# Kernel optimization log

Measured on AMD Instinct MI355X. Metric: run time of the kernel, lower is better.

Reference implementation:

```python
import jax, jax.numpy as jnp
import numpy as np

N_NODES = 10000
N_EDGES = 160000
B = 128
HEADS = 4
DIMS = [36, 128, 256, 512]
NEG_SLOPE = 0.2  # PyG GATConv default


def setup_inputs() -> dict:
    key = jax.random.key(0)
    ks = jax.random.split(key, 32)
    inp = {}
    inp["x"] = jax.random.normal(ks[0], (N_NODES, DIMS[0]), jnp.float32)
    inp["edge_index"] = jax.random.randint(ks[1], (2, N_EDGES), 0, N_NODES)
    inp["batch"] = jnp.sort(jax.random.randint(ks[2], (N_NODES,), 0, B))
    ki = 3
    for i in range(3):
        din, dout = DIMS[i], DIMS[i + 1]
        C = dout // HEADS
        inp[f"gcn_w{i}"] = jax.random.normal(ks[ki], (din, dout), jnp.float32) * (din ** -0.5); ki += 1
        inp[f"gcn_b{i}"] = jnp.zeros((dout,), jnp.float32)
        inp[f"gat_w{i}"] = jax.random.normal(ks[ki], (dout, dout), jnp.float32) * (dout ** -0.5); ki += 1
        inp[f"gat_as{i}"] = jax.random.normal(ks[ki], (HEADS, C), jnp.float32) * 0.1; ki += 1
        inp[f"gat_ad{i}"] = jax.random.normal(ks[ki], (HEADS, C), jnp.float32) * 0.1; ki += 1
        inp[f"gat_b{i}"] = jnp.zeros((dout,), jnp.float32)
    D = DIMS[-1]
    inp["ap_w1"] = jax.random.normal(ks[ki], (D, D // 2), jnp.float32) * (D ** -0.5); ki += 1
    inp["ap_b1"] = jnp.zeros((D // 2,), jnp.float32)
    inp["ap_w2"] = jax.random.normal(ks[ki], (D // 2, 1), jnp.float32) * ((D // 2) ** -0.5); ki += 1
    inp["ap_b2"] = jnp.zeros((1,), jnp.float32)
    return inp


def _gcn(x, w, b, src, dst, n):
    # PyG GCNConv: add self-loops, symmetric deg^-1/2 normalization, bias after agg
    h = x @ w  # [N, dout]
    deg = jax.ops.segment_sum(jnp.ones_like(dst, dtype=h.dtype), dst, n) + 1.0  # incl. self-loop
    dinv = deg ** -0.5
    norm = dinv[src] * dinv[dst]  # [E]
    agg = jax.ops.segment_sum(h[src] * norm[:, None], dst, n)
    agg = agg + h * (dinv * dinv)[:, None]  # self-loop messages
    return agg + b


def _gat(x, w, a_s, a_d, b, src, dst, n):
    # PyG GATConv: self-loops, leaky-relu logits, segment softmax over dst, concat heads
    C = w.shape[1] // HEADS
    h = (x @ w).reshape(n, HEADS, C)
    alpha_src = (h * a_s).sum(-1)  # [N, H]
    alpha_dst = (h * a_d).sum(-1)  # [N, H]
    loop = jnp.arange(n)
    s = jnp.concatenate([src, loop])
    d = jnp.concatenate([dst, loop])
    e = jax.nn.leaky_relu(alpha_src[s] + alpha_dst[d], NEG_SLOPE)  # [E+N, H]
    m = jax.ops.segment_max(e, d, n)
    ex = jnp.exp(e - m[d])
    den = jax.ops.segment_sum(ex, d, n)
    alpha = ex / den[d]  # [E+N, H]
    out = jax.ops.segment_sum(h[s] * alpha[:, :, None], d, n)  # [N, H, C]
    return out.reshape(n, HEADS * C) + b


def _forward(x, edge_index, batch, params, ap_w1, ap_b1, ap_w2, ap_b2):
    src, dst = edge_index[0], edge_index[1]
    n = x.shape[0]
    x_in = x
    n_layers = len(params)
    for i, (gw, gb, aw, a_s, a_d, ab) in enumerate(params):
        h = jax.nn.relu(_gcn(x, gw, gb, src, dst, n))  # dropout is identity in eval
        x = h + _gat(h, aw, a_s, a_d, ab, src, dst, n)
        if i < n_layers - 1:
            if x.shape[-1] == x_in.shape[-1]:
                x = x + x_in
            x_in = x
    # attention pooling (global softmax then per-graph masked renorm)
    a = jnp.tanh(x @ ap_w1 + ap_b1) @ ap_w2 + ap_b2  # [N, 1]
    a = jax.nn.softmax(a, axis=0)
    mask = jax.nn.one_hot(batch, B, dtype=x.dtype)  # [N, B]
    aw_ = a * mask
    aw_ = aw_ / (aw_.sum(0, keepdims=True) + 1e-8)
    graph_emb = aw_.T @ x  # [B, D]
    cnt = jax.ops.segment_sum(jnp.ones((n,), x.dtype), batch, B)
    ssum = jax.ops.segment_sum(x, batch, B)
    mean = ssum / jnp.maximum(cnt, 1.0)[:, None]
    smax = jax.ops.segment_max(x, batch, B)
    return jnp.concatenate([graph_emb, mean, smax, ssum], axis=1)  # [B, 4*D]


def reference(x, edge_index, batch,
              gcn_w0, gcn_b0, gat_w0, gat_as0, gat_ad0, gat_b0,
              gcn_w1, gcn_b1, gat_w1, gat_as1, gat_ad1, gat_b1,
              gcn_w2, gcn_b2, gat_w2, gat_as2, gat_ad2, gat_b2,
              ap_w1, ap_b1, ap_w2, ap_b2):
    params = [
        (gcn_w0, gcn_b0, gat_w0, gat_as0, gat_ad0, gat_b0),
        (gcn_w1, gcn_b1, gat_w1, gat_as1, gat_ad1, gat_b1),
        (gcn_w2, gcn_b2, gat_w2, gat_as2, gat_ad2, gat_b2),
    ]
    return _forward(x, edge_index, batch, params, ap_w1, ap_b1, ap_w2, ap_b2)
```

## Files before the change

### kernel.cpp

```cpp
#include <hip/hip_runtime.h>
#include <math.h>

#define NN 10000
#define NE 160000
#define NB 128
#define NH 4
#define DOUT 512
#define NEG 0.2f
#define CNT_BLKS ((NE + 255) / 256)

typedef __attribute__((ext_vector_type(8))) short short8;
typedef __attribute__((ext_vector_type(4))) float f32x4;
typedef __attribute__((ext_vector_type(4))) unsigned short us4;

__device__ __forceinline__ float leakyf(float v){ return v > 0.f ? v : NEG*v; }
__device__ __forceinline__ void fma4(float4& a, const float4 v, float w){
  a.x += v.x*w; a.y += v.y*w; a.z += v.z*w; a.w += v.w*w;
}
__device__ __forceinline__ void mul4(float4& a, float s){
  a.x *= s; a.y *= s; a.z *= s; a.w *= s;
}
__device__ __forceinline__ unsigned short f2bf(float f){
  unsigned int u = __float_as_uint(f);
  u += 0x7FFFu + ((u >> 16) & 1u);
  return (unsigned short)(u >> 16);
}
__device__ __forceinline__ float bf2f(unsigned short h){
  return __uint_as_float(((unsigned int)h) << 16);
}
__device__ __forceinline__ void split2(float v, unsigned short& h, unsigned short& l){
  h = f2bf(v);
  l = f2bf(v - bf2f(h));
}
__device__ __forceinline__ void store_hl(unsigned short* H, unsigned short* L,
                                         size_t base, float4 v){
  us4 h, l; unsigned short hh, ll;
  split2(v.x, hh, ll); h[0]=hh; l[0]=ll;
  split2(v.y, hh, ll); h[1]=hh; l[1]=ll;
  split2(v.z, hh, ll); h[2]=hh; l[2]=ll;
  split2(v.w, hh, ll); h[3]=hh; l[3]=ll;
  *(us4*)&H[base] = h;
  *(us4*)&L[base] = l;
}
__device__ __forceinline__ float4 load_hl(const unsigned short* __restrict__ H,
                                          const unsigned short* __restrict__ L, size_t base){
  us4 h = *(const us4*)&H[base];
  us4 l = *(const us4*)&L[base];
  return make_float4(bf2f(h[0])+bf2f(l[0]), bf2f(h[1])+bf2f(l[1]),
                     bf2f(h[2])+bf2f(l[2]), bf2f(h[3])+bf2f(l[3]));
}
__device__ __forceinline__ void gl_lds16(const unsigned short* g, unsigned short* l){
  __builtin_amdgcn_global_load_lds(
      (const __attribute__((address_space(1))) unsigned int*)g,
      (__attribute__((address_space(3))) unsigned int*)l, 16, 0, 0);
}

struct AllConv {
  const float* src[7];
  unsigned short* dh[7];
  unsigned short* dl[7];
  int K[7], Mm[7], Kp[7], tot[7];
};

__global__ void k_count_conv(const int* __restrict__ dst, int* __restrict__ cnt,
                             AllConv a, int convTot){
  int bid = blockIdx.x;
  if (bid < CNT_BLKS){
    int e = bid*256 + threadIdx.x;
    if (e < NE) atomicAdd(&cnt[dst[e]], 1);
  } else {
    int idx = (bid - CNT_BLKS)*256 + threadIdx.x;
    if (idx >= convTot) return;
    int j = 0;
    while (idx >= a.tot[j]){ idx -= a.tot[j]; j++; }
    int Kp = a.Kp[j], K = a.K[j], M = a.Mm[j];
    int kk = idx % Kp, m = idx / Kp;
    float v = (kk < K) ? a.src[j][(size_t)kk*M + m] : 0.f;
    unsigned short h, l; split2(v, h, l);
    a.dh[j][idx] = h; a.dl[j][idx] = l;
  }
}

__global__ __launch_bounds__(1024) void k_scan_all(
    const int* __restrict__ cnt, const int* __restrict__ batch,
    int* __restrict__ rowptr, float* __restrict__ dinv,
    int* __restrict__ cursor, float* __restrict__ apre,
    int* __restrict__ starts){
  __shared__ int sh[NN];
  __shared__ int pref[1024];
  int t = threadIdx.x;
  for (int i = t; i < NN; i += 1024) sh[i] = cnt[i];
  if (t <= NB){
    int lo = 0, hi = NN;
    while (lo < hi){ int mid = (lo + hi) >> 1; if (batch[mid] < t) lo = mid + 1; else hi = mid; }
    starts[t] = lo;
  }
  __syncthreads();
  int base = t*10;
  int csum = 0;
#pragma unroll
  for (int k = 0; k < 10; k++){ int i = base + k; if (i < NN) csum += sh[i]; }
  pref[t] = csum; __syncthreads();
  for (int o = 1; o < 1024; o <<= 1){
    int v = (t >= o) ? pref[t - o] : 0;
    __syncthreads();
    pref[t] += v;
    __syncthreads();
  }
  int run = pref[t] - csum;
#pragma unroll
  for (int k = 0; k < 10; k++){
    int i = base + k;
    if (i < NN){
      int c = sh[i];
      rowptr[i] = run;
      run += c;
      dinv[i] = rsqrtf((float)c + 1.f);
      cursor[i] = 0;
      apre[i] = 0.f;
    }
  }
  if (t == 1023) rowptr[NN] = pref[1023];
}

__global__ void k_fill(const int* __restrict__ src, const int* __restrict__ dst,
                       const int* __restrict__ rowptr, int* __restrict__ cursor,
                       int* __restrict__ colidx){
  int e = blockIdx.x*blockDim.x + threadIdx.x;
  if (e >= NE) return;
  int d = dst[e];
  int pos = atomicAdd(&cursor[d], 1);
  colidx[rowptr[d] + pos] = src[e];
}

#define GBM 64
#define GBN 128
#define GBK 64
__global__ __launch_bounds__(256) void k_gemm_bf3(
    const unsigned short* __restrict__ Ah, const unsigned short* __restrict__ Al,
    const unsigned short* __restrict__ Bh, const unsigned short* __restrict__ Bl,
    float* __restrict__ C, int N, int Kp, int M, int mode,
    const float* __restrict__ bias, unsigned short* __restrict__ outH,
    unsigned short* __restrict__ outL,
    const float* __restrict__ a_s, const float* __restrict__ a_d,
    float* __restrict__ as_o, float* __restrict__ ad_o, int Cdim){
  __shared__ unsigned short AsH[2*GBM*32], AsL[2*GBM*32];
  __shared__ unsigned short BsH[2*GBN*32], BsL[2*GBN*32];
  __shared__ float sred[2][GBM][4];
  int gx = M / GBN;
  int gy = (N + GBM - 1) / GBM;
  const int G = 8;
  int bid = blockIdx.x;
  int full = gy / G;
  int bid_full = full * G * gx;
  int by, bx;
  if (bid < bid_full){
    int g = bid / (G*gx); int rem = bid % (G*gx);
    by = g*G + rem % G; bx = rem / G;
  } else {
    int rem = bid - bid_full; int rows = gy - full*G;
    by = full*G + rem % rows; bx = rem / rows;
  }
  int row0 = by * GBM, col0 = bx * GBN;
  int t = threadIdx.x;
  int w = t >> 6, L = t & 63;
  int lm = L & 15, lq = L >> 4;
  int wc = w * 32;

  int sr = L >> 2, sc = L & 3;
  int art = w*16 + sr;
  int ga  = (sc - ((art >> 1) & 3)) & 3;
  int agrow = min(row0 + art, N-1);
  int brt0 = w*16 + sr;
  int brt1 = (w+4)*16 + sr;
  int gb0 = (sc - ((brt0 >> 1) & 3)) & 3;
  int gb1 = (sc - ((brt1 >> 1) & 3)) & 3;
  int bgrow0 = col0 + brt0, bgrow1 = col0 + brt1;

  int rc = (lq + (lm >> 1)) & 3;
  int aoff[4], boff[2];
#pragma unroll
  for (int mi = 0; mi < 4; mi++) aoff[mi] = (mi*16 + lm)*32 + rc*8;
#pragma unroll
  for (int ni = 0; ni < 2; ni++) boff[ni] = (wc + ni*16 + lm)*32 + rc*8;

  f32x4 acc[4][2];
#pragma unroll
  for (int i = 0; i < 4; i++)
#pragma unroll
    for (int j = 0; j < 2; j++) acc[i][j] = (f32x4){0.f,0.f,0.f,0.f};

  int nk = Kp / GBK;
  for (int kt = 0; kt < nk; kt++){
    int k0 = kt * GBK;
    if (kt) __syncthreads();
#pragma unroll
    for (int h = 0; h < 2; h++){
      int kh = k0 + h*32;
      gl_lds16(&Ah[(size_t)agrow*Kp + kh + ga*8],  &AsH[h*2048 + w*512]);
      gl_lds16(&Al[(size_t)agrow*Kp + kh + ga*8],  &AsL[h*2048 + w*512]);
      gl_lds16(&Bh[(size_t)bgrow0*Kp + kh + gb0*8], &BsH[h*4096 + w*512]);
      gl_lds16(&Bh[(size_t)bgrow1*Kp + kh + gb1*8], &BsH[h*4096 + (w+4)*512]);
      gl_lds16(&Bl[(size_t)bgrow0*Kp + kh + gb0*8], &BsL[h*4096 + w*512]);
      gl_lds16(&Bl[(size_t)bgrow1*Kp + kh + gb1*8], &BsL[h*4096 + (w+4)*512]);
    }
    __syncthreads();

#pragma unroll
    for (int h = 0; h < 2; h++){
      short8 ah[4], al[4], bh[2], bl[2];
#pragma unroll
      for (int mi = 0; mi < 4; mi++){
        ah[mi] = *(const short8*)&AsH[h*2048 + aoff[mi]];
        al[mi] = *(const short8*)&AsL[h*2048 + aoff[mi]];
      }
#pragma unroll
      for (int ni = 0; ni < 2; ni++){
        bh[ni] = *(const short8*)&BsH[h*4096 + boff[ni]];
        bl[ni] = *(const short8*)&BsL[h*4096 + boff[ni]];
      }
#pragma unroll
      for (int mi = 0; mi < 4; mi++)
#pragma unroll
        for (int ni = 0; ni < 2; ni++){
          acc[mi][ni] = __builtin_amdgcn_mfma_f32_16x16x32_bf16(ah[mi], bh[ni], acc[mi][ni], 0, 0, 0);
          acc[mi][ni] = __builtin_amdgcn_mfma_f32_16x16x32_bf16(ah[mi], bl[ni], acc[mi][ni], 0, 0, 0);
          acc[mi][ni] = __builtin_amdgcn_mfma_f32_16x16x32_bf16(al[mi], bh[ni], acc[mi][ni], 0, 0, 0);
        }
    }
  }
  if (mode == 1){
#pragma unroll
    for (int mi = 0; mi < 4; mi++)
#pragma unroll
      for (int ni = 0; ni < 2; ni++){
#pragma unroll
        for (int r = 0; r < 4; r++){
          int row = row0 + mi*16 + lq*4 + r;
          int col = col0 + wc + ni*16 + lm;
          if (row < N){
            float v = fmaxf(acc[mi][ni][r] + bias[col], 0.f);
            unsigned short hh, ll; split2(v, hh, ll);
            outH[(size_t)row*M + col] = hh;
            outL[(size_t)row*M + col] = ll;
          }
        }
      }
  } else if (mode != 3){
#pragma unroll
    for (int mi = 0; mi < 4; mi++)
#pragma unroll
      for (int ni = 0; ni < 2; ni++){
#pragma unroll
        for (int r = 0; r < 4; r++){
          int row = row0 + mi*16 + lq*4 + r;
          int col = col0 + wc + ni*16 + lm;
          if (row < N) C[(size_t)row*M + col] = acc[mi][ni][r];
        }
      }
  }
  if (mode == 2){
    float sA0 = a_s[col0 + wc + lm], sA1 = a_s[col0 + wc + 16 + lm];
    float dA0 = a_d[col0 + wc + lm], dA1 = a_d[col0 + wc + 16 + lm];
#pragma unroll
    for (int mi = 0; mi < 4; mi++)
#pragma unroll
      for (int r = 0; r < 4; r++){
        float vs = acc[mi][0][r]*sA0 + acc[mi][1][r]*sA1;
        float vd = acc[mi][0][r]*dA0 + acc[mi][1][r]*dA1;
#pragma unroll
        for (int o = 1; o <= 8; o <<= 1){
          vs += __shfl_xor(vs, o);
          vd += __shfl_xor(vd, o);
        }
        if (lm == 0){
          int row = mi*16 + lq*4 + r;
          sred[0][row][w] = vs;
          sred[1][row][w] = vd;
        }
      }
    __syncthreads();
    if (t < GBM){
      int n = row0 + t;
      if (n < N){
        int wph = Cdim >> 5;
        int nheads = 4 / wph;
        for (int g = 0; g < nheads; g++){
          float ss = 0.f, dd = 0.f;
          for (int q = 0; q < wph; q++){
            ss += sred[0][t][g*wph + q];
            dd += sred[1][t][g*wph + q];
          }
          int hd = (col0 + g*wph*32) / Cdim;
          as_o[n*NH + hd] = ss;
          ad_o[n*NH + hd] = dd;
        }
      }
    }
  } else if (mode == 3){
    float b0 = bias[col0 + wc + lm], b1v = bias[col0 + wc + 16 + lm];
    float w0v = a_s[col0 + wc + lm], w1v = a_s[col0 + wc + 16 + lm];
#pragma unroll
    for (int mi = 0; mi < 4; mi++)
#pragma unroll
      for (int r = 0; r < 4; r++){
        float v = tanhf(acc[mi][0][r] + b0)*w0v + tanhf(acc[mi][1][r] + b1v)*w1v;
#pragma unroll
        for (int o = 1; o <= 8; o <<= 1) v += __shfl_xor(v, o);
        if (lm == 0) sred[0][mi*16 + lq*4 + r][w] = v;
      }
    __syncthreads();
    if (t < GBM){
      int n = row0 + t;
      if (n < N){
        float s = sred[0][t][0] + sred[0][t][1] + sred[0][t][2] + sred[0][t][3];
        atomicAdd(&as_o[n], s);
      }
    }
  }
}

__global__ __launch_bounds__(256) void k_gcn_pre0(
    const float* __restrict__ x0, const float* __restrict__ dinv,
    const int* __restrict__ rowptr, const int* __restrict__ colidx,
    unsigned short* __restrict__ outH, unsigned short* __restrict__ outL){
  int t = threadIdx.x;
  int sub = t & 15;
  int n = blockIdx.x*16 + (t >> 4);
  if (n >= NN) return;
  int f0 = sub*4;
  bool act = f0 < 36;
  int b = rowptr[n], e = rowptr[n+1];
  float dn = dinv[n];
  float4 a0 = make_float4(0,0,0,0), a1 = make_float4(0,0,0,0);
  float4 a2 = make_float4(0,0,0,0), a3 = make_float4(0,0,0,0);
  if (act){
    float4 sv = *(const float4*)&x0[(size_t)n*36 + f0];
    int j = b;
    for (; j + 7 < e; j += 8){
      int s0 = colidx[j],   s1 = colidx[j+1], s2 = colidx[j+2], s3 = colidx[j+3];
      int s4 = colidx[j+4], s5 = colidx[j+5], s6 = colidx[j+6], s7 = colidx[j+7];
      float w0 = dinv[s0], w1 = dinv[s1], w2 = dinv[s2], w3 = dinv[s3];
      float w4 = dinv[s4], w5 = dinv[s5], w6 = dinv[s6], w7 = dinv[s7];
      float4 v0 = *(const float4*)&x0[(size_t)s0*36 + f0];
      float4 v1 = *(const float4*)&x0[(size_t)s1*36 + f0];
      float4 v2 = *(const float4*)&x0[(size_t)s2*36 + f0];
      float4 v3 = *(const float4*)&x0[(size_t)s3*36 + f0];
      float4 v4 = *(const float4*)&x0[(size_t)s4*36 + f0];
      float4 v5 = *(const float4*)&x0[(size_t)s5*36 + f0];
      float4 v6 = *(const float4*)&x0[(size_t)s6*36 + f0];
      float4 v7 = *(const float4*)&x0[(size_t)s7*36 + f0];
      fma4(a0, v0, w0*dn); fma4(a1, v1, w1*dn);
      fma4(a2, v2, w2*dn); fma4(a3, v3, w3*dn);
      fma4(a0, v4, w4*dn); fma4(a1, v5, w5*dn);
      fma4(a2, v6, w6*dn); fma4(a3, v7, w7*dn);
    }
    for (; j + 3 < e; j += 4){
      int s0 = colidx[j], s1 = colidx[j+1], s2 = colidx[j+2], s3 = colidx[j+3];
      float w0 = dinv[s0], w1 = dinv[s1], w2 = dinv[s2], w3 = dinv[s3];
      float4 v0 = *(const float4*)&x0[(size_t)s0*36 + f0];
      float4 v1 = *(const float4*)&x0[(size_t)s1*36 + f0];
      float4 v2 = *(const float4*)&x0[(size_t)s2*36 + f0];
      float4 v3 = *(const float4*)&x0[(size_t)s3*36 + f0];
      fma4(a0, v0, w0*dn); fma4(a1, v1, w1*dn);
      fma4(a2, v2, w2*dn); fma4(a3, v3, w3*dn);
    }
    for (; j < e; j++){
      int s = colidx[j];
      float4 v = *(const float4*)&x0[(size_t)s*36 + f0];
      fma4(a0, v, dinv[s]*dn);
    }
    float4 acc = make_float4(a0.x+a1.x+a2.x+a3.x, a0.y+a1.y+a2.y+a3.y,
                             a0.z+a1.z+a2.z+a3.z, a0.w+a1.w+a2.w+a3.w);
    float dn2 = dn*dn;
    acc.x += sv.x*dn2; acc.y += sv.y*dn2; acc.z += sv.z*dn2; acc.w += sv.w*dn2;
    store_hl(outH, outL, (size_t)n*64 + f0, acc);
  } else {
    store_hl(outH, outL, (size_t)n*64 + f0, make_float4(0,0,0,0));
  }
}

__global__ __launch_bounds__(256) void k_gcn_pre(
    const unsigned short* __restrict__ inH, const unsigned short* __restrict__ inL,
    const float* __restrict__ dinv,
    const int* __restrict__ rowptr, const int* __restrict__ colidx,
    unsigned short* __restrict__ outH, unsigned short* __restrict__ outL,
    int Kp, int nchunk){
  int bid = blockIdx.x;
  int chunk = bid % nchunk, grp = bid / nchunk;
  int t = threadIdx.x;
  int sub = t & 15;
  int n = grp*16 + (t >> 4);
  if (n >= NN) return;
  int f0 = chunk*64 + sub*4;
  int b = rowptr[n], e = rowptr[n+1];
  float dn = dinv[n];
  float4 sv = load_hl(inH, inL, (size_t)n*Kp + f0);
  float4 a0 = make_float4(0,0,0,0), a1 = make_float4(0,0,0,0);
  float4 a2 = make_float4(0,0,0,0), a3 = make_float4(0,0,0,0);
  int j = b;
  for (; j + 7 < e; j += 8){
    int s0 = colidx[j],   s1 = colidx[j+1], s2 = colidx[j+2], s3 = colidx[j+3];
    int s4 = colidx[j+4], s5 = colidx[j+5], s6 = colidx[j+6], s7 = colidx[j+7];
    float w0 = dinv[s0], w1 = dinv[s1], w2 = dinv[s2], w3 = dinv[s3];
    float w4 = dinv[s4], w5 = dinv[s5], w6 = dinv[s6], w7 = dinv[s7];
    float4 v0 = load_hl(inH, inL, (size_t)s0*Kp + f0);
    float4 v1 = load_hl(inH, inL, (size_t)s1*Kp + f0);
    float4 v2 = load_hl(inH, inL, (size_t)s2*Kp + f0);
    float4 v3 = load_hl(inH, inL, (size_t)s3*Kp + f0);
    float4 v4 = load_hl(inH, inL, (size_t)s4*Kp + f0);
    float4 v5 = load_hl(inH, inL, (size_t)s5*Kp + f0);
    float4 v6 = load_hl(inH, inL, (size_t)s6*Kp + f0);
    float4 v7 = load_hl(inH, inL, (size_t)s7*Kp + f0);
    fma4(a0, v0, w0*dn); fma4(a1, v1, w1*dn);
    fma4(a2, v2, w2*dn); fma4(a3, v3, w3*dn);
    fma4(a0, v4, w4*dn); fma4(a1, v5, w5*dn);
    fma4(a2, v6, w6*dn); fma4(a3, v7, w7*dn);
  }
  for (; j + 3 < e; j += 4){
    int s0 = colidx[j], s1 = colidx[j+1], s2 = colidx[j+2], s3 = colidx[j+3];
    float w0 = dinv[s0], w1 = dinv[s1], w2 = dinv[s2], w3 = dinv[s3];
    float4 v0 = load_hl(inH, inL, (size_t)s0*Kp + f0);
    float4 v1 = load_hl(inH, inL, (size_t)s1*Kp + f0);
    float4 v2 = load_hl(inH, inL, (size_t)s2*Kp + f0);
    float4 v3 = load_hl(inH, inL, (size_t)s3*Kp + f0);
    fma4(a0, v0, w0*dn); fma4(a1, v1, w1*dn);
    fma4(a2, v2, w2*dn); fma4(a3, v3, w3*dn);
  }
  for (; j < e; j++){
    int s = colidx[j];
    float4 v = load_hl(inH, inL, (size_t)s*Kp + f0);
    fma4(a0, v, dinv[s]*dn);
  }
  float4 acc = make_float4(a0.x+a1.x+a2.x+a3.x, a0.y+a1.y+a2.y+a3.y,
                           a0.z+a1.z+a2.z+a3.z, a0.w+a1.w+a2.w+a3.w);
  float dn2 = dn*dn;
  acc.x += sv.x*dn2; acc.y += sv.y*dn2; acc.z += sv.z*dn2; acc.w += sv.w*dn2;
  store_hl(outH, outL, (size_t)n*Kp + f0, acc);
}

__global__ __launch_bounds__(256) void k_gat_gather(
    const float* __restrict__ hg,
    const unsigned short* __restrict__ inH, const unsigned short* __restrict__ inL,
    const int* __restrict__ rowptr, const int* __restrict__ colidx,
    const float* __restrict__ as_, const float* __restrict__ ad_,
    const float* __restrict__ ab,
    unsigned short* __restrict__ outH, unsigned short* __restrict__ outL,
    int M, int C, int nchunk){
  int bid = blockIdx.x;
  int chunk = bid % nchunk, grp = bid / nchunk;
  int t = threadIdx.x;
  int sub = t & 15;
  int n = grp*16 + (t >> 4);
  if (n >= NN) return;
  int f0 = chunk*64 + sub*4;
  int hd = f0 / C;
  int b = rowptr[n], e = rowptr[n+1];
  int ai = n*NH + hd;
  float adn = ad_[ai];
  float selflog = leakyf(as_[ai] + adn);
  float4 sv = *(const float4*)&hg[(size_t)n*M + f0];
  float4 hv = load_hl(inH, inL, (size_t)n*M + f0);
  float4 bb = *(const float4*)&ab[f0];
  float m = selflog, d = 1.f;
  float4 a0 = make_float4(0,0,0,0), a1 = make_float4(0,0,0,0);
  float4 a2 = make_float4(0,0,0,0), a3 = make_float4(0,0,0,0);
  int j = b;
  for (; j + 7 < e; j += 8){
    int s0 = colidx[j],   s1 = colidx[j+1], s2 = colidx[j+2], s3 = colidx[j+3];
    int s4 = colidx[j+4], s5 = colidx[j+5], s6 = colidx[j+6], s7 = colidx[j+7];
    float l0 = leakyf(as_[s0*NH + hd] + adn), l1 = leakyf(as_[s1*NH + hd] + adn);
    float l2 = leakyf(as_[s2*NH + hd] + adn), l3 = leakyf(as_[s3*NH + hd] + adn);
    float l4 = leakyf(as_[s4*NH + hd] + adn), l5 = leakyf(as_[s5*NH + hd] + adn);
    float l6 = leakyf(as_[s6*NH + hd] + adn), l7 = leakyf(as_[s7*NH + hd] + adn);
    float4 v0 = *(const float4*)&hg[(size_t)s0*M + f0];
    float4 v1 = *(const float4*)&hg[(size_t)s1*M + f0];
    float4 v2 = *(const float4*)&hg[(size_t)s2*M + f0];
    float4 v3 = *(const float4*)&hg[(size_t)s3*M + f0];
    float4 v4 = *(const float4*)&hg[(size_t)s4*M + f0];
    float4 v5 = *(const float4*)&hg[(size_t)s5*M + f0];
    float4 v6 = *(const float4*)&hg[(size_t)s6*M + f0];
    float4 v7 = *(const float4*)&hg[(size_t)s7*M + f0];
    float m8 = fmaxf(fmaxf(fmaxf(l0, l1), fmaxf(l2, l3)),
                     fmaxf(fmaxf(l4, l5), fmaxf(l6, l7)));
    if (m8 > m){
      float sc = expf(m - m8);
      d *= sc; mul4(a0, sc); mul4(a1, sc); mul4(a2, sc); mul4(a3, sc);
      m = m8;
    }
    float w0 = expf(l0 - m), w1 = expf(l1 - m);
    float w2 = expf(l2 - m), w3 = expf(l3 - m);
    float w4 = expf(l4 - m), w5 = expf(l5 - m);
    float w6 = expf(l6 - m), w7 = expf(l7 - m);
    d += ((w0 + w1) + (w2 + w3)) + ((w4 + w5) + (w6 + w7));
    fma4(a0, v0, w0); fma4(a1, v1, w1);
    fma4(a2, v2, w2); fma4(a3, v3, w3);
    fma4(a0, v4, w4); fma4(a1, v5, w5);
    fma4(a2, v6, w6); fma4(a3, v7, w7);
  }
  for (; j + 3 < e; j += 4){
    int s0 = colidx[j], s1 = colidx[j+1], s2 = colidx[j+2], s3 = colidx[j+3];
    float l0 = leakyf(as_[s0*NH + hd] + adn), l1 = leakyf(as_[s1*NH + hd] + adn);
    float l2 = leakyf(as_[s2*NH + hd] + adn), l3 = leakyf(as_[s3*NH + hd] + adn);
    float4 v0 = *(const float4*)&hg[(size_t)s0*M + f0];
    float4 v1 = *(const float4*)&hg[(size_t)s1*M + f0];
    float4 v2 = *(const float4*)&hg[(size_t)s2*M + f0];
    float4 v3 = *(const float4*)&hg[(size_t)s3*M + f0];
    float m4 = fmaxf(fmaxf(l0, l1), fmaxf(l2, l3));
    if (m4 > m){
      float sc = expf(m - m4);
      d *= sc; mul4(a0, sc); mul4(a1, sc); mul4(a2, sc); mul4(a3, sc);
      m = m4;
    }
    float w0 = expf(l0 - m), w1 = expf(l1 - m);
    float w2 = expf(l2 - m), w3 = expf(l3 - m);
    d += (w0 + w1) + (w2 + w3);
    fma4(a0, v0, w0); fma4(a1, v1, w1);
    fma4(a2, v2, w2); fma4(a3, v3, w3);
  }
  for (; j < e; j++){
    int s = colidx[j];
    float l = leakyf(as_[s*NH + hd] + adn);
    float4 v = *(const float4*)&hg[(size_t)s*M + f0];
    if (l > m){
      float sc = expf(m - l);
      d *= sc; mul4(a0, sc); mul4(a1, sc); mul4(a2, sc); mul4(a3, sc);
      m = l;
    }
    float ww = expf(l - m);
    d += ww;
    fma4(a0, v, ww);
  }
  float4 acc = make_float4(a0.x+a1.x+a2.x+a3.x, a0.y+a1.y+a2.y+a3.y,
                           a0.z+a1.z+a2.z+a3.z, a0.w+a1.w+a2.w+a3.w);
  float es = expf(selflog - m), inv = 1.f/d;
  float4 r = make_float4(
    hv.x + bb.x + (sv.x*es + acc.x)*inv,
    hv.y + bb.y + (sv.y*es + acc.y)*inv,
    hv.z + bb.z + (sv.z*es + acc.z)*inv,
    hv.w + bb.w + (sv.w*es + acc.w)*inv);
  store_hl(outH, outL, (size_t)n*M + f0, r);
}

__global__ __launch_bounds__(512) void k_pool(
    const unsigned short* __restrict__ xH, const unsigned short* __restrict__ xL,
    const float* __restrict__ apre, const int* __restrict__ starts,
    float* __restrict__ out){
  __shared__ float red[512];
  __shared__ float4 comb[3][4][128];
  int g = blockIdx.x, t = threadIdx.x;
  int b = starts[g], e = starts[g+1];
  float m = -INFINITY;
  for (int n = b + t; n < e; n += 512) m = fmaxf(m, apre[n]);
  red[t] = m; __syncthreads();
  for (int o = 256; o > 0; o >>= 1){
    if (t < o) red[t] = fmaxf(red[t], red[t + o]);
    __syncthreads();
  }
  m = red[0]; __syncthreads();
  float s = 0.f;
  for (int n = b + t; n < e; n += 512) s += expf(apre[n] - m);
  red[t] = s; __syncthreads();
  for (int o = 256; o > 0; o >>= 1){
    if (t < o) red[t] += red[t + o];
    __syncthreads();
  }
  float inv = 1.f / (red[0] + 1e-8f);
  int lf = t & 127, sl = t >> 7;
  float4 sum = make_float4(0,0,0,0), wacc = make_float4(0,0,0,0);
  float4 mx = make_float4(-INFINITY,-INFINITY,-INFINITY,-INFINITY);
  for (int n = b + sl; n < e; n += 4){
    float4 xv = load_hl(xH, xL, (size_t)n*DOUT + lf*4);
    float p = expf(apre[n] - m) * inv;
    sum.x += xv.x; sum.y += xv.y; sum.z += xv.z; sum.w += xv.w;
    mx.x = fmaxf(mx.x, xv.x); mx.y = fmaxf(mx.y, xv.y);
    mx.z = fmaxf(mx.z, xv.z); mx.w = fmaxf(mx.w, xv.w);
    fma4(wacc, xv, p);
  }
  comb[0][sl][lf] = wacc; comb[1][sl][lf] = sum; comb[2][sl][lf] = mx;
  __syncthreads();
  if (sl == 0){
#pragma unroll
    for (int q = 1; q < 4; q++){
      float4 w2 = comb[0][q][lf], s2 = comb[1][q][lf], m2 = comb[2][q][lf];
      wacc.x += w2.x; wacc.y += w2.y; wacc.z += w2.z; wacc.w += w2.w;
      sum.x += s2.x; sum.y += s2.y; sum.z += s2.z; sum.w += s2.w;
      mx.x = fmaxf(mx.x, m2.x); mx.y = fmaxf(mx.y, m2.y);
      mx.z = fmaxf(mx.z, m2.z); mx.w = fmaxf(mx.w, m2.w);
    }
    float ic = 1.f / fmaxf((float)(e - b), 1.f);
    float4* o = (float4*)(out + (size_t)g*4*DOUT);
    o[lf]       = wacc;
    o[128 + lf] = make_float4(sum.x*ic, sum.y*ic, sum.z*ic, sum.w*ic);
    o[256 + lf] = mx;
    o[384 + lf] = sum;
  }
}

extern "C" void kernel_launch(void* const* d_in, const int* in_sizes, int n_in,
                              void* d_out, int out_size, void* d_ws, size_t ws_size,
                              hipStream_t stream) {
  const float* x0   = (const float*)d_in[0];
  const int*   ei   = (const int*)d_in[1];
  const int*   src  = ei;
  const int*   dst  = ei + NE;
  const int*   batch= (const int*)d_in[2];
  const float* gw[3]  = {(const float*)d_in[3],  (const float*)d_in[9],  (const float*)d_in[15]};
  const float* gb[3]  = {(const float*)d_in[4],  (const float*)d_in[10], (const float*)d_in[16]};
  const float* aw[3]  = {(const float*)d_in[5],  (const float*)d_in[11], (const float*)d_in[17]};
  const float* asw[3] = {(const float*)d_in[6],  (const float*)d_in[12], (const float*)d_in[18]};
  const float* adw[3] = {(const float*)d_in[7],  (const float*)d_in[13], (const float*)d_in[19]};
  const float* ab[3]  = {(const float*)d_in[8],  (const float*)d_in[14], (const float*)d_in[20]};
  const float* apw1 = (const float*)d_in[21];
  const float* apb1 = (const float*)d_in[22];
  const float* apw2 = (const float*)d_in[23];
  float* out = (float*)d_out;

  char* p = (char*)d_ws;
  auto alloc = [&](size_t bytes) -> void* {
    void* r = (void*)p; p += (bytes + 255) & ~(size_t)255; return r;
  };
  float* f1 = (float*)alloc((size_t)NN*512*4);
  unsigned short* actH0 = (unsigned short*)alloc((size_t)NN*512*2);
  unsigned short* actL0 = (unsigned short*)alloc((size_t)NN*512*2);
  unsigned short* actH1 = (unsigned short*)alloc((size_t)NN*512*2);
  unsigned short* actL1 = (unsigned short*)alloc((size_t)NN*512*2);
  unsigned short* preH  = (unsigned short*)alloc((size_t)NN*256*2);
  unsigned short* preL  = (unsigned short*)alloc((size_t)NN*256*2);
  const int wK[7]  = {36, 128, 128, 256, 256, 512, 512};
  const int wM[7]  = {128, 128, 256, 256, 512, 512, 256};
  const int wKp[7] = {64, 128, 128, 256, 256, 512, 512};
  const float* wsrc[7] = {gw[0], aw[0], gw[1], aw[1], gw[2], aw[2], apw1};
  unsigned short* wTh[7]; unsigned short* wTl[7];
  for (int i = 0; i < 7; i++){
    size_t sz = (size_t)wM[i]*wKp[i]*2;
    wTh[i] = (unsigned short*)alloc(sz);
    wTl[i] = (unsigned short*)alloc(sz);
  }
  float* dinv = (float*)alloc(NN*4);
  float* as_  = (float*)alloc(NN*NH*4);
  float* ad_  = (float*)alloc(NN*NH*4);
  float* apre = (float*)alloc(NN*4);
  int* rowptr = (int*)alloc((NN+1)*4);
  int* colidx = (int*)alloc((size_t)NE*4);
  int* cnt    = (int*)alloc(NN*4);
  int* cursor = (int*)alloc(NN*4);
  int* starts = (int*)alloc((NB+1)*4);

  AllConv ac;
  int convTot = 0;
  for (int i = 0; i < 7; i++){
    ac.src[i] = wsrc[i]; ac.dh[i] = wTh[i]; ac.dl[i] = wTl[i];
    ac.K[i] = wK[i]; ac.Mm[i] = wM[i]; ac.Kp[i] = wKp[i];
    ac.tot[i] = wKp[i]*wM[i];
    convTot += ac.tot[i];
  }

  hipMemsetAsync(cnt, 0, NN*sizeof(int), stream);
  int convBlks = (convTot + 255) / 256;
  k_count_conv<<<CNT_BLKS + convBlks, 256, 0, stream>>>(dst, cnt, ac, convTot);
  k_scan_all<<<1, 1024, 0, stream>>>(cnt, batch, rowptr, dinv, cursor, apre, starts);
  k_fill<<<(NE+255)/256, 256, 0, stream>>>(src, dst, rowptr, cursor, colidx);

  const int dims[4] = {36, 128, 256, 512};
  const int ngrp = (NN + 15) / 16;
  const unsigned short* curH = nullptr; const unsigned short* curL = nullptr;
  int wi = 0;
  for (int i = 0; i < 3; i++){
    int Kin = (i == 0) ? 64 : dims[i];
    int M = dims[i+1], C = M/NH;
    int nchunk_in = Kin / 64;
    int nchunk = M / 64;
    int nblk = (M/GBN) * ((NN+GBM-1)/GBM);
    if (i == 0){
      k_gcn_pre0<<<ngrp, 256, 0, stream>>>(x0, dinv, rowptr, colidx, preH, preL);
    } else {
      k_gcn_pre<<<nchunk_in*ngrp, 256, 0, stream>>>(curH, curL, dinv, rowptr, colidx,
                                                    preH, preL, Kin, nchunk_in);
    }
    k_gemm_bf3<<<nblk, 256, 0, stream>>>(preH, preL, wTh[wi], wTl[wi], f1, NN, wKp[wi], M,
                                         1, gb[i], actH0, actL0,
                                         nullptr, nullptr, nullptr, nullptr, C);
    wi++;
    k_gemm_bf3<<<nblk, 256, 0, stream>>>(actH0, actL0, wTh[wi], wTl[wi], f1, NN, wKp[wi], M,
                                         2, nullptr, nullptr, nullptr,
                                         asw[i], adw[i], as_, ad_, C);
    wi++;
    k_gat_gather<<<nchunk*ngrp, 256, 0, stream>>>(f1, actH0, actL0, rowptr, colidx,
                                                  as_, ad_, ab[i],
                                                  actH1, actL1, M, C, nchunk);
    curH = actH1; curL = actL1;
  }

  {
    int nblk = (256/GBN) * ((NN+GBM-1)/GBM);
    k_gemm_bf3<<<nblk, 256, 0, stream>>>(actH1, actL1, wTh[6], wTl[6], f1, NN, wKp[6], 256,
                                         3, apb1, nullptr, nullptr,
                                         apw2, nullptr, apre, nullptr, 64);
  }
  k_pool<<<NB, 512, 0, stream>>>(actH1, actL1, apre, starts, out);
}
```

Before: 394.5 us.

## Keep fp32 activation copies for gathers and drop online-max softmax rescaling

```diff
diff --git a/kernel.cpp b/kernel.cpp
--- a/kernel.cpp
+++ b/kernel.cpp
@@ -13,12 +13,9 @@
 typedef __attribute__((ext_vector_type(4))) float f32x4;
 typedef __attribute__((ext_vector_type(4))) unsigned short us4;
 
-__device__ __forceinline__ float leakyf(float v){ return v > 0.f ? v : NEG*v; }
+__device__ __forceinline__ float leakyf(float v){ return fmaxf(v, NEG*v); }
 __device__ __forceinline__ void fma4(float4& a, const float4 v, float w){
   a.x += v.x*w; a.y += v.y*w; a.z += v.z*w; a.w += v.w*w;
-}
-__device__ __forceinline__ void mul4(float4& a, float s){
-  a.x *= s; a.y *= s; a.z *= s; a.w *= s;
 }
 __device__ __forceinline__ unsigned short f2bf(float f){
   unsigned int u = __float_as_uint(f);
@@ -41,13 +38,6 @@
   split2(v.w, hh, ll); h[3]=hh; l[3]=ll;
   *(us4*)&H[base] = h;
   *(us4*)&L[base] = l;
-}
-__device__ __forceinline__ float4 load_hl(const unsigned short* __restrict__ H,
-                                          const unsigned short* __restrict__ L, size_t base){
-  us4 h = *(const us4*)&H[base];
-  us4 l = *(const us4*)&L[base];
-  return make_float4(bf2f(h[0])+bf2f(l[0]), bf2f(h[1])+bf2f(l[1]),
-                     bf2f(h[2])+bf2f(l[2]), bf2f(h[3])+bf2f(l[3]));
 }
 __device__ __forceinline__ void gl_lds16(const unsigned short* g, unsigned short* l){
   __builtin_amdgcn_global_load_lds(
@@ -243,6 +233,7 @@
             unsigned short hh, ll; split2(v, hh, ll);
             outH[(size_t)row*M + col] = hh;
             outL[(size_t)row*M + col] = ll;
+            C[(size_t)row*M + col] = v;
           }
         }
       }
@@ -381,8 +372,7 @@
 }
 
 __global__ __launch_bounds__(256) void k_gcn_pre(
-    const unsigned short* __restrict__ inH, const unsigned short* __restrict__ inL,
-    const float* __restrict__ dinv,
+    const float* __restrict__ xf, const float* __restrict__ dinv,
     const int* __restrict__ rowptr, const int* __restrict__ colidx,
     unsigned short* __restrict__ outH, unsigned short* __restrict__ outL,
     int Kp, int nchunk){
@@ -395,7 +385,7 @@
   int f0 = chunk*64 + sub*4;
   int b = rowptr[n], e = rowptr[n+1];
   float dn = dinv[n];
-  float4 sv = load_hl(inH, inL, (size_t)n*Kp + f0);
+  float4 sv = *(const float4*)&xf[(size_t)n*Kp + f0];
   float4 a0 = make_float4(0,0,0,0), a1 = make_float4(0,0,0,0);
   float4 a2 = make_float4(0,0,0,0), a3 = make_float4(0,0,0,0);
   int j = b;
@@ -404,14 +394,14 @@
     int s4 = colidx[j+4], s5 = colidx[j+5], s6 = colidx[j+6], s7 = colidx[j+7];
     float w0 = dinv[s0], w1 = dinv[s1], w2 = dinv[s2], w3 = dinv[s3];
     float w4 = dinv[s4], w5 = dinv[s5], w6 = dinv[s6], w7 = dinv[s7];
-    float4 v0 = load_hl(inH, inL, (size_t)s0*Kp + f0);
-    float4 v1 = load_hl(inH, inL, (size_t)s1*Kp + f0);
-    float4 v2 = load_hl(inH, inL, (size_t)s2*Kp + f0);
-    float4 v3 = load_hl(inH, inL, (size_t)s3*Kp + f0);
-    float4 v4 = load_hl(inH, inL, (size_t)s4*Kp + f0);
-    float4 v5 = load_hl(inH, inL, (size_t)s5*Kp + f0);
-    float4 v6 = load_hl(inH, inL, (size_t)s6*Kp + f0);
-    float4 v7 = load_hl(inH, inL, (size_t)s7*Kp + f0);
+    float4 v0 = *(const float4*)&xf[(size_t)s0*Kp + f0];
+    float4 v1 = *(const float4*)&xf[(size_t)s1*Kp + f0];
+    float4 v2 = *(const float4*)&xf[(size_t)s2*Kp + f0];
+    float4 v3 = *(const float4*)&xf[(size_t)s3*Kp + f0];
+    float4 v4 = *(const float4*)&xf[(size_t)s4*Kp + f0];
+    float4 v5 = *(const float4*)&xf[(size_t)s5*Kp + f0];
+    float4 v6 = *(const float4*)&xf[(size_t)s6*Kp + f0];
+    float4 v7 = *(const float4*)&xf[(size_t)s7*Kp + f0];
     fma4(a0, v0, w0*dn); fma4(a1, v1, w1*dn);
     fma4(a2, v2, w2*dn); fma4(a3, v3, w3*dn);
     fma4(a0, v4, w4*dn); fma4(a1, v5, w5*dn);
@@ -420,16 +410,16 @@
   for (; j + 3 < e; j += 4){
     int s0 = colidx[j], s1 = colidx[j+1], s2 = colidx[j+2], s3 = colidx[j+3];
     float w0 = dinv[s0], w1 = dinv[s1], w2 = dinv[s2], w3 = dinv[s3];
-    float4 v0 = load_hl(inH, inL, (size_t)s0*Kp + f0);
-    float4 v1 = load_hl(inH, inL, (size_t)s1*Kp + f0);
-    float4 v2 = load_hl(inH, inL, (size_t)s2*Kp + f0);
-    float4 v3 = load_hl(inH, inL, (size_t)s3*Kp + f0);
+    float4 v0 = *(const float4*)&xf[(size_t)s0*Kp + f0];
+    float4 v1 = *(const float4*)&xf[(size_t)s1*Kp + f0];
+    float4 v2 = *(const float4*)&xf[(size_t)s2*Kp + f0];
+    float4 v3 = *(const float4*)&xf[(size_t)s3*Kp + f0];
     fma4(a0, v0, w0*dn); fma4(a1, v1, w1*dn);
     fma4(a2, v2, w2*dn); fma4(a3, v3, w3*dn);
   }
   for (; j < e; j++){
     int s = colidx[j];
-    float4 v = load_hl(inH, inL, (size_t)s*Kp + f0);
+    float4 v = *(const float4*)&xf[(size_t)s*Kp + f0];
     fma4(a0, v, dinv[s]*dn);
   }
   float4 acc = make_float4(a0.x+a1.x+a2.x+a3.x, a0.y+a1.y+a2.y+a3.y,
@@ -440,12 +430,12 @@
 }
 
 __global__ __launch_bounds__(256) void k_gat_gather(
-    const float* __restrict__ hg,
-    const unsigned short* __restrict__ inH, const unsigned short* __restrict__ inL,
+    const float* __restrict__ hg, const float* __restrict__ hf,
     const int* __restrict__ rowptr, const int* __restrict__ colidx,
     const float* __restrict__ as_, const float* __restrict__ ad_,
     const float* __restrict__ ab,
     unsigned short* __restrict__ outH, unsigned short* __restrict__ outL,
+    float* __restrict__ xf,
     int M, int C, int nchunk){
   int bid = blockIdx.x;
   int chunk = bid % nchunk, grp = bid / nchunk;
@@ -458,11 +448,12 @@
   int b = rowptr[n], e = rowptr[n+1];
   int ai = n*NH + hd;
   float adn = ad_[ai];
-  float selflog = leakyf(as_[ai] + adn);
+  float sl = fminf(fmaxf(leakyf(as_[ai] + adn), -80.f), 80.f);
+  float es = __expf(sl);
   float4 sv = *(const float4*)&hg[(size_t)n*M + f0];
-  float4 hv = load_hl(inH, inL, (size_t)n*M + f0);
+  float4 hv = *(const float4*)&hf[(size_t)n*M + f0];
   float4 bb = *(const float4*)&ab[f0];
-  float m = selflog, d = 1.f;
+  float d = es;
   float4 a0 = make_float4(0,0,0,0), a1 = make_float4(0,0,0,0);
   float4 a2 = make_float4(0,0,0,0), a3 = make_float4(0,0,0,0);
   int j = b;
@@ -481,69 +472,38 @@
     float4 v5 = *(const float4*)&hg[(size_t)s5*M + f0];
     float4 v6 = *(const float4*)&hg[(size_t)s6*M + f0];
     float4 v7 = *(const float4*)&hg[(size_t)s7*M + f0];
-    float m8 = fmaxf(fmaxf(fmaxf(l0, l1), fmaxf(l2, l3)),
-                     fmaxf(fmaxf(l4, l5), fmaxf(l6, l7)));
-    if (m8 > m){
-      float sc = expf(m - m8);
-      d *= sc; mul4(a0, sc); mul4(a1, sc); mul4(a2, sc); mul4(a3, sc);
-      m = m8;
-    }
-    float w0 = expf(l0 - m), w1 = expf(l1 - m);
-    float w2 = expf(l2 - m), w3 = expf(l3 - m);
-    float w4 = expf(l4 - m), w5 = expf(l5 - m);
-    float w6 = expf(l6 - m), w7 = expf(l7 - m);
+    float w0 = __expf(fminf(fmaxf(l0,-80.f),80.f)), w1 = __expf(fminf(fmaxf(l1,-80.f),80.f));
+    float w2 = __expf(fminf(fmaxf(l2,-80.f),80.f)), w3 = __expf(fminf(fmaxf(l3,-80.f),80.f));
+    float w4 = __expf(fminf(fmaxf(l4,-80.f),80.f)), w5 = __expf(fminf(fmaxf(l5,-80.f),80.f));
+    float w6 = __expf(fminf(fmaxf(l6,-80.f),80.f)), w7 = __expf(fminf(fmaxf(l7,-80.f),80.f));
     d += ((w0 + w1) + (w2 + w3)) + ((w4 + w5) + (w6 + w7));
     fma4(a0, v0, w0); fma4(a1, v1, w1);
     fma4(a2, v2, w2); fma4(a3, v3, w3);
     fma4(a0, v4, w4); fma4(a1, v5, w5);
     fma4(a2, v6, w6); fma4(a3, v7, w7);
   }
-  for (; j + 3 < e; j += 4){
-    int s0 = colidx[j], s1 = colidx[j+1], s2 = colidx[j+2], s3 = colidx[j+3];
-    float l0 = leakyf(as_[s0*NH + hd] + adn), l1 = leakyf(as_[s1*NH + hd] + adn);
-    float l2 = leakyf(as_[s2*NH + hd] + adn), l3 = leakyf(as_[s3*NH + hd] + adn);
-    float4 v0 = *(const float4*)&hg[(size_t)s0*M + f0];
-    float4 v1 = *(const float4*)&hg[(size_t)s1*M + f0];
-    float4 v2 = *(const float4*)&hg[(size_t)s2*M + f0];
-    float4 v3 = *(const float4*)&hg[(size_t)s3*M + f0];
-    float m4 = fmaxf(fmaxf(l0, l1), fmaxf(l2, l3));
-    if (m4 > m){
-      float sc = expf(m - m4);
-      d *= sc; mul4(a0, sc); mul4(a1, sc); mul4(a2, sc); mul4(a3, sc);
-      m = m4;
-    }
-    float w0 = expf(l0 - m), w1 = expf(l1 - m);
-    float w2 = expf(l2 - m), w3 = expf(l3 - m);
-    d += (w0 + w1) + (w2 + w3);
-    fma4(a0, v0, w0); fma4(a1, v1, w1);
-    fma4(a2, v2, w2); fma4(a3, v3, w3);
-  }
   for (; j < e; j++){
     int s = colidx[j];
     float l = leakyf(as_[s*NH + hd] + adn);
     float4 v = *(const float4*)&hg[(size_t)s*M + f0];
-    if (l > m){
-      float sc = expf(m - l);
-      d *= sc; mul4(a0, sc); mul4(a1, sc); mul4(a2, sc); mul4(a3, sc);
-      m = l;
-    }
-    float ww = expf(l - m);
+    float ww = __expf(fminf(fmaxf(l,-80.f),80.f));
     d += ww;
     fma4(a0, v, ww);
   }
   float4 acc = make_float4(a0.x+a1.x+a2.x+a3.x, a0.y+a1.y+a2.y+a3.y,
                            a0.z+a1.z+a2.z+a3.z, a0.w+a1.w+a2.w+a3.w);
-  float es = expf(selflog - m), inv = 1.f/d;
+  float inv = 1.f/d;
   float4 r = make_float4(
     hv.x + bb.x + (sv.x*es + acc.x)*inv,
     hv.y + bb.y + (sv.y*es + acc.y)*inv,
     hv.z + bb.z + (sv.z*es + acc.z)*inv,
     hv.w + bb.w + (sv.w*es + acc.w)*inv);
+  *(float4*)&xf[(size_t)n*M + f0] = r;
   store_hl(outH, outL, (size_t)n*M + f0, r);
 }
 
 __global__ __launch_bounds__(512) void k_pool(
-    const unsigned short* __restrict__ xH, const unsigned short* __restrict__ xL,
+    const float* __restrict__ xf,
     const float* __restrict__ apre, const int* __restrict__ starts,
     float* __restrict__ out){
   __shared__ float red[512];
@@ -559,7 +519,7 @@
   }
   m = red[0]; __syncthreads();
   float s = 0.f;
-  for (int n = b + t; n < e; n += 512) s += expf(apre[n] - m);
+  for (int n = b + t; n < e; n += 512) s += __expf(apre[n] - m);
   red[t] = s; __syncthreads();
   for (int o = 256; o > 0; o >>= 1){
     if (t < o) red[t] += red[t + o];
@@ -570,8 +530,8 @@
   float4 sum = make_float4(0,0,0,0), wacc = make_float4(0,0,0,0);
   float4 mx = make_float4(-INFINITY,-INFINITY,-INFINITY,-INFINITY);
   for (int n = b + sl; n < e; n += 4){
-    float4 xv = load_hl(xH, xL, (size_t)n*DOUT + lf*4);
-    float p = expf(apre[n] - m) * inv;
+    float4 xv = *(const float4*)&xf[(size_t)n*DOUT + lf*4];
+    float p = __expf(apre[n] - m) * inv;
     sum.x += xv.x; sum.y += xv.y; sum.z += xv.z; sum.w += xv.w;
     mx.x = fmaxf(mx.x, xv.x); mx.y = fmaxf(mx.y, xv.y);
     mx.z = fmaxf(mx.z, xv.z); mx.w = fmaxf(mx.w, xv.w);
@@ -621,6 +581,8 @@
     void* r = (void*)p; p += (bytes + 255) & ~(size_t)255; return r;
   };
   float* f1 = (float*)alloc((size_t)NN*512*4);
+  float* hf = (float*)alloc((size_t)NN*512*4);
+  float* xf = (float*)alloc((size_t)NN*512*4);
   unsigned short* actH0 = (unsigned short*)alloc((size_t)NN*512*2);
   unsigned short* actL0 = (unsigned short*)alloc((size_t)NN*512*2);
   unsigned short* actH1 = (unsigned short*)alloc((size_t)NN*512*2);
@@ -664,7 +626,6 @@
 
   const int dims[4] = {36, 128, 256, 512};
   const int ngrp = (NN + 15) / 16;
-  const unsigned short* curH = nullptr; const unsigned short* curL = nullptr;
   int wi = 0;
   for (int i = 0; i < 3; i++){
     int Kin = (i == 0) ? 64 : dims[i];
@@ -675,10 +636,10 @@
     if (i == 0){
       k_gcn_pre0<<<ngrp, 256, 0, stream>>>(x0, dinv, rowptr, colidx, preH, preL);
     } else {
-      k_gcn_pre<<<nchunk_in*ngrp, 256, 0, stream>>>(curH, curL, dinv, rowptr, colidx,
+      k_gcn_pre<<<nchunk_in*ngrp, 256, 0, stream>>>(xf, dinv, rowptr, colidx,
                                                     preH, preL, Kin, nchunk_in);
     }
-    k_gemm_bf3<<<nblk, 256, 0, stream>>>(preH, preL, wTh[wi], wTl[wi], f1, NN, wKp[wi], M,
+    k_gemm_bf3<<<nblk, 256, 0, stream>>>(preH, preL, wTh[wi], wTl[wi], hf, NN, wKp[wi], M,
                                          1, gb[i], actH0, actL0,
                                          nullptr, nullptr, nullptr, nullptr, C);
     wi++;
@@ -686,17 +647,16 @@
                                          2, nullptr, nullptr, nullptr,
                                          asw[i], adw[i], as_, ad_, C);
     wi++;
-    k_gat_gather<<<nchunk*ngrp, 256, 0, stream>>>(f1, actH0, actL0, rowptr, colidx,
+    k_gat_gather<<<nchunk*ngrp, 256, 0, stream>>>(f1, hf, rowptr, colidx,
                                                   as_, ad_, ab[i],
-                                                  actH1, actL1, M, C, nchunk);
-    curH = actH1; curL = actL1;
+                                                  actH1, actL1, xf, M, C, nchunk);
   }
 
   {
     int nblk = (256/GBN) * ((NN+GBM-1)/GBM);
-    k_gemm_bf3<<<nblk, 256, 0, stream>>>(actH1, actL1, wTh[6], wTl[6], f1, NN, wKp[6], 256,
+    k_gemm_bf3<<<nblk, 256, 0, stream>>>(actH1, actL1, wTh[6], wTl[6], nullptr, NN, wKp[6], 256,
                                          3, apb1, nullptr, nullptr,
                                          apw2, nullptr, apre, nullptr, 64);
   }
-  k_pool<<<NB, 512, 0, stream>>>(actH1, actL1, apre, starts, out);
-}
+  k_pool<<<NB, 512, 0, stream>>>(xf, apre, starts, out);
+}
```

Result: faster. 382.1 us (-3.1%).
